# Performance work log

Hardware: AMD Instinct MI355X
Metric: run time of the kernel (lower is better)

Reference implementation:

```python
import jax, jax.numpy as jnp
import numpy as np

IN_CH, OUT_CH, K = 3, 16, 3

def setup_inputs() -> dict:
    key = jax.random.key(0)
    kx, kw, kb = jax.random.split(key, 3)
    x = jax.random.normal(kx, (64, IN_CH, 256, 256), dtype=jnp.float32)
    # kaiming_uniform_(a=sqrt(5)) -> bound = sqrt(6 / ((1+5) * fan_in)) = 1/sqrt(fan_in)
    fan_in = IN_CH * K * K
    bound = 1.0 / np.sqrt(fan_in)
    weight = jax.random.uniform(kw, (OUT_CH, IN_CH, K, K), dtype=jnp.float32,
                                minval=-bound, maxval=bound)
    bias = jax.random.uniform(kb, (OUT_CH,), dtype=jnp.float32,
                              minval=-bound, maxval=bound)
    return {"x": x, "weight": weight, "bias": bias}

def reference(x, weight, bias):
    # stride 1, VALID padding conv2d (NCHW / OIHW), same math as the quadruple loop
    out = jax.lax.conv_general_dilated(
        x, weight,
        window_strides=(1, 1),
        padding="VALID",
        dimension_numbers=("NCHW", "OIHW", "NCHW"),
    )
    return out + bias[None, :, None, None]
```

## Files before the change

### kernel.cpp

```cpp
#include <hip/hip_runtime.h>


constexpr int N = 64, C = 3, H = 256, W = 256;
constexpr int OC = 16, K = 3, OH = 254, OW = 254;
constexpr int PW = OW / 2;

__global__ __launch_bounds__(256) void conv3x3_kernel(
    const float* __restrict__ x, const float* __restrict__ w,
    const float* __restrict__ bias, float* __restrict__ out)
{
    int idx = blockIdx.x * blockDim.x + threadIdx.x;
    constexpr int total = N * OH * PW;
    if (idx >= total) return;

    int pw = idx % PW;
    int t  = idx / PW;
    int oh = t % OH;
    int n  = t / OH;
    int ow = pw * 2;

    float acc0[OC], acc1[OC];
    #pragma unroll
    for (int oc = 0; oc < OC; ++oc) {
        float b = bias[oc];
        acc0[oc] = b;
        acc1[oc] = b;
    }

    const float* xb = x + (size_t)n * C * H * W;

    #pragma unroll
    for (int c = 0; c < C; ++c) {
        #pragma unroll
        for (int kh = 0; kh < K; ++kh) {
            const float* xr = xb + ((size_t)c * H + (oh + kh)) * W + ow;
            float i0 = xr[0], i1 = xr[1], i2 = xr[2], i3 = xr[3];
            #pragma unroll
            for (int oc = 0; oc < OC; ++oc) {
                float w0 = w[((oc * C + c) * K + kh) * K + 0];
                float w1 = w[((oc * C + c) * K + kh) * K + 1];
                float w2 = w[((oc * C + c) * K + kh) * K + 2];
                acc0[oc] += i0 * w0 + i1 * w1 + i2 * w2;
                acc1[oc] += i1 * w0 + i2 * w1 + i3 * w2;
            }
        }
    }

    float* ob = out + ((size_t)n * OC * OH + oh) * OW + ow;
    #pragma unroll
    for (int oc = 0; oc < OC; ++oc) {
        float2 v = make_float2(acc0[oc], acc1[oc]);
        *reinterpret_cast<float2*>(ob + (size_t)oc * OH * OW) = v;
    }
}

extern "C" void kernel_launch(void* const* d_in, const int* in_sizes, int n_in,
                              void* d_out, int out_size, void* d_ws, size_t ws_size,
                              hipStream_t stream) {
    const float* x    = (const float*)d_in[0];
    const float* w    = (const float*)d_in[1];
    const float* bias = (const float*)d_in[2];
    float* out        = (float*)d_out;

    constexpr int total  = N * OH * PW;
    constexpr int block  = 256;
    constexpr int blocks = (total + block - 1) / block;
    conv3x3_kernel<<<blocks, block, 0, stream>>>(x, w, bias, out);
}
```

Measured before the change: 330.6 us.

## Stage weights in LDS and tile 8 pixels by 4 channels per thread

Weights and bias are transposed into shared memory so a float4 read yields four output channels per tap. Each thread now computes 8 consecutive output pixels for a group of 4 output channels, using vectorized float4 input loads. This replaces repeated scalar global weight reads and raises arithmetic reuse per loaded input. In exchange, each input row is loaded by four channel-group threads, and boundary handling relies on zero-padding the last reads and guarding stores.

```diff
diff --git a/kernel.cpp b/kernel.cpp
--- a/kernel.cpp
+++ b/kernel.cpp
@@ -3,54 +3,83 @@
 
 constexpr int N = 64, C = 3, H = 256, W = 256;
 constexpr int OC = 16, K = 3, OH = 254, OW = 254;
-constexpr int PW = OW / 2;
+constexpr int PX = 8;
+constexpr int NWU = 32;
+constexpr int NG = 4;
 
 __global__ __launch_bounds__(256) void conv3x3_kernel(
     const float* __restrict__ x, const float* __restrict__ w,
     const float* __restrict__ bias, float* __restrict__ out)
 {
-    int idx = blockIdx.x * blockDim.x + threadIdx.x;
-    constexpr int total = N * OH * PW;
-    if (idx >= total) return;
+    __shared__ float lw[C * K * K * OC + OC];
+    int t = threadIdx.x;
+    for (int i = t; i < C * K * K * OC; i += 256) {
+        int oc = i & 15, r = i >> 4;
+        int kw = r % 3, kh = (r / 3) % 3, c = r / 9;
+        lw[i] = w[oc * 27 + c * 9 + kh * 3 + kw];
+    }
+    if (t < OC) lw[C * K * K * OC + t] = bias[t];
+    __syncthreads();
 
-    int pw = idx % PW;
-    int t  = idx / PW;
-    int oh = t % OH;
-    int n  = t / OH;
-    int ow = pw * 2;
+    int idx = blockIdx.x * 256 + t;
+    int owu = idx & (NWU - 1);
+    int g   = (idx >> 5) & (NG - 1);
+    int rr  = idx >> 7;
+    int oh  = rr % OH;
+    int n   = rr / OH;
+    int ow0 = owu * PX;
 
-    float acc0[OC], acc1[OC];
-    #pragma unroll
-    for (int oc = 0; oc < OC; ++oc) {
-        float b = bias[oc];
-        acc0[oc] = b;
-        acc1[oc] = b;
+    float accv[PX][4];
+    {
+        const float* bv = &lw[C * K * K * OC + 4 * g];
+        float b0 = bv[0], b1 = bv[1], b2 = bv[2], b3 = bv[3];
+        #pragma unroll
+        for (int j = 0; j < PX; ++j) {
+            accv[j][0] = b0; accv[j][1] = b1; accv[j][2] = b2; accv[j][3] = b3;
+        }
     }
 
-    const float* xb = x + (size_t)n * C * H * W;
+    const float* xb = x + ((size_t)n * C * H + oh) * W + ow0;
+    bool full = (ow0 + 10 <= W);
 
     #pragma unroll
     for (int c = 0; c < C; ++c) {
         #pragma unroll
         for (int kh = 0; kh < K; ++kh) {
-            const float* xr = xb + ((size_t)c * H + (oh + kh)) * W + ow;
-            float i0 = xr[0], i1 = xr[1], i2 = xr[2], i3 = xr[3];
+            const float* xr = xb + ((size_t)c * H + kh) * W;
+            float4 xa = *reinterpret_cast<const float4*>(xr);
+            float4 xc = *reinterpret_cast<const float4*>(xr + 4);
+            float x8 = full ? xr[8] : 0.f;
+            float x9 = full ? xr[9] : 0.f;
+            float xx[10] = {xa.x, xa.y, xa.z, xa.w, xc.x, xc.y, xc.z, xc.w, x8, x9};
+
+            const float* wp = &lw[(c * 9 + kh * 3) * 16 + 4 * g];
             #pragma unroll
-            for (int oc = 0; oc < OC; ++oc) {
-                float w0 = w[((oc * C + c) * K + kh) * K + 0];
-                float w1 = w[((oc * C + c) * K + kh) * K + 1];
-                float w2 = w[((oc * C + c) * K + kh) * K + 2];
-                acc0[oc] += i0 * w0 + i1 * w1 + i2 * w2;
-                acc1[oc] += i1 * w0 + i2 * w1 + i3 * w2;
+            for (int kw = 0; kw < K; ++kw) {
+                float4 wv = *reinterpret_cast<const float4*>(wp + kw * 16);
+                #pragma unroll
+                for (int j = 0; j < PX; ++j) {
+                    float xi = xx[j + kw];
+                    accv[j][0] += xi * wv.x;
+                    accv[j][1] += xi * wv.y;
+                    accv[j][2] += xi * wv.z;
+                    accv[j][3] += xi * wv.w;
+                }
             }
         }
     }
 
-    float* ob = out + ((size_t)n * OC * OH + oh) * OW + ow;
+    float* ob = out + ((size_t)(n * OC + g * 4) * OH + oh) * OW + ow0;
     #pragma unroll
-    for (int oc = 0; oc < OC; ++oc) {
-        float2 v = make_float2(acc0[oc], acc1[oc]);
-        *reinterpret_cast<float2*>(ob + (size_t)oc * OH * OW) = v;
+    for (int q = 0; q < 4; ++q) {
+        float* oq = ob + (size_t)q * OH * OW;
+        #pragma unroll
+        for (int p = 0; p < 4; ++p) {
+            if (ow0 + 2 * p < OW) {
+                float2 v = make_float2(accv[2 * p][q], accv[2 * p + 1][q]);
+                *reinterpret_cast<float2*>(oq + 2 * p) = v;
+            }
+        }
     }
 }
 
@@ -62,8 +91,8 @@
     const float* bias = (const float*)d_in[2];
     float* out        = (float*)d_out;
 
-    constexpr int total  = N * OH * PW;
+    constexpr int total  = N * OH * NG * NWU;
     constexpr int block  = 256;
-    constexpr int blocks = (total + block - 1) / block;
+    constexpr int blocks = total / block;
     conv3x3_kernel<<<blocks, block, 0, stream>>>(x, w, bias, out);
 }
```

Measured after the change: 429.3 us. 1.3x slower.
